# Optimization experiments

Hardware: AMD Instinct MI355X
Metric: run time of the kernel (lower is better)

## Reference

```python
import jax, jax.numpy as jnp
import numpy as np

TMSG = 15  # max_len - 1


def setup_inputs() -> dict:
    key = jax.random.key(0)
    ks = jax.random.split(key, 8)
    B, T_in, E, H, V = 4096, 4, 256, 512, 32000
    s = lambda k, shape: jax.random.normal(k, shape, jnp.float32) * 0.05
    return {
        "inp": jax.random.normal(ks[0], (B, T_in, E), jnp.float32),
        "Wx0": s(ks[1], (E, 4 * H)),
        "Wh0": s(ks[2], (H, 4 * H)),
        "b0": jnp.zeros((4 * H,), jnp.float32),
        "Wx1": s(ks[3], (H, 4 * H)),
        "Wh1": s(ks[4], (H, 4 * H)),
        "b1": jnp.zeros((4 * H,), jnp.float32),
        "Wd": s(ks[5], (H, V)),
        "bd": jnp.zeros((V,), jnp.float32),
    }


def _lstm_step(x, h, c, Wx, Wh, b):
    # Keras LSTMCell gate order: i, f, g(cell), o
    z = x @ Wx + h @ Wh + b
    i, f, g, o = jnp.split(z, 4, axis=-1)
    c = jax.nn.sigmoid(f) * c + jax.nn.sigmoid(i) * jnp.tanh(g)
    h = jax.nn.sigmoid(o) * jnp.tanh(c)
    return h, c


def reference(inp, Wx0, Wh0, b0, Wx1, Wh1, b1, Wd, bd):
    B = inp.shape[0]
    H = Wh0.shape[0]
    z = jnp.zeros((B, H), inp.dtype)

    def scan_fn(carry, x_t):
        h0, c0, h1, c1 = carry
        h0, c0 = _lstm_step(x_t, h0, c0, Wx0, Wh0, b0)
        h1, c1 = _lstm_step(h0, h1, c1, Wx1, Wh1, b1)
        return (h0, c0, h1, c1), None

    # NOTE: source bug resets initial_state to None every step, so each of the
    # max_len-1 steps runs the identical stacked LSTM from zero state; we run it once.
    (h0, c0, h1, c1), _ = jax.lax.scan(scan_fn, (z, z, z, z), jnp.swapaxes(inp, 0, 1))
    out = h1  # (B, H) last-step output of top cell

    log_probs = jax.nn.log_softmax(out @ Wd + bd, axis=-1)  # (B, V)
    probs = jnp.exp(log_probs)
    entropy = -jnp.sum(probs * log_probs, axis=-1)  # (B,)

    keys = jax.random.split(jax.random.key(42), TMSG)
    samples = jax.vmap(lambda k: jax.random.categorical(k, log_probs, axis=-1))(keys)  # (T, B)
    lp = log_probs[jnp.arange(B)[None, :], samples]  # (T, B) log_prob of sampled chars
    ent = jnp.broadcast_to(entropy[None], (TMSG, B))  # (T, B)

    message = samples.T  # (B, T)
    message = jnp.concatenate([message, jnp.zeros_like(message)], axis=1)  # (B, 2T)
    state_h = jnp.stack([h0, c0])  # keras unpack quirk: states[0] = [h, c] of cell 0
    return (message, lp, ent, state_h)
```

## Files before the change

### kernel.cpp

```cpp
#include <hip/hip_runtime.h>
#include <stdint.h>
#include <math.h>

#define BB 4096
#define HH 512
#define VV 32000
#define NT 15
#define STF 2097152
#define NXT 250

struct KeysArg { uint32_t w[2*NT]; };

__host__ __device__ inline void tf2x32(uint32_t k0, uint32_t k1,
                                       uint32_t x0, uint32_t x1,
                                       uint32_t& o0, uint32_t& o1) {
  uint32_t ks2 = k0 ^ k1 ^ 0x1BD11BDAu;
  x0 += k0; x1 += k1;
#define TF_R(r) { x0 += x1; x1 = (x1 << (r)) | (x1 >> (32 - (r))); x1 ^= x0; }
  TF_R(13) TF_R(15) TF_R(26) TF_R(6)
  x0 += k1; x1 += ks2 + 1u;
  TF_R(17) TF_R(29) TF_R(16) TF_R(24)
  x0 += ks2; x1 += k0 + 2u;
  TF_R(13) TF_R(15) TF_R(26) TF_R(6)
  x0 += k0; x1 += k1 + 3u;
  TF_R(17) TF_R(29) TF_R(16) TF_R(24)
  x0 += k1; x1 += ks2 + 4u;
  TF_R(13) TF_R(15) TF_R(26) TF_R(6)
  x0 += ks2; x1 += k0 + 5u;
#undef TF_R
  o0 = x0; o1 = x1;
}

__device__ inline void gll16(const float* g, float* l) {
  __builtin_amdgcn_global_load_lds(
      (const __attribute__((address_space(1))) void*)g,
      (__attribute__((address_space(3))) void*)l, 16, 0, 0);
}

__global__ __launch_bounds__(256)
void gemm_sk(const float* __restrict__ A0, int lda0,
             const float* __restrict__ W0, int koff0, int Klen0,
             const float* __restrict__ A1, int lda1,
             const float* __restrict__ W1, int koff1, int Klen1,
             int ldw,
             const float* __restrict__ bias,
             float* __restrict__ C0, float* __restrict__ C1, int ldc)
{
  const float* A; const float* W; float* C; int lda, koff, Klen;
  if (blockIdx.z == 0) { A = A0; lda = lda0; W = W0; koff = koff0; Klen = Klen0; C = C0; }
  else                 { A = A1; lda = lda1; W = W1; koff = koff1; Klen = Klen1; C = C1; }

  __shared__ float As[2][128 * 16];
  __shared__ float Ws[2][16 * 128];
  const int tid = threadIdx.x;
  const int lane = tid & 63, wv = tid >> 6;
  const int m0 = blockIdx.y * 128;
  const int n0 = blockIdx.x * 128;
  const int tx = tid & 15, ty = tid >> 4;

  float acc[8][8];
  #pragma unroll
  for (int i = 0; i < 8; ++i)
    #pragma unroll
    for (int j = 0; j < 8; ++j) acc[i][j] = 0.0f;

  const int a_row_in = (lane >> 2);
  const int a_chunk  = (lane & 3) * 4;
  const int w_row_in = (lane >> 5);
  const int w_col    = (lane & 31) * 4;

  auto STAGE = [&](int buf, int kt) {
    const int k0 = koff + (kt << 4);
    #pragma unroll
    for (int i = 0; i < 2; ++i) {
      const int seg = wv * 2 + i;
      gll16(A + (size_t)(m0 + seg * 16 + a_row_in) * lda + (k0 + a_chunk),
            &As[buf][seg * 256]);
      gll16(W + (size_t)(k0 + seg * 2 + w_row_in) * ldw + (n0 + w_col),
            &Ws[buf][seg * 256]);
    }
  };

  const int nkt = Klen >> 4;
  STAGE(0, 0);
  asm volatile("s_waitcnt vmcnt(0)" ::: "memory");
  __syncthreads();

  int cur = 0;
  for (int kt = 0; kt < nkt; ++kt) {
    if (kt + 1 < nkt) STAGE(cur ^ 1, kt + 1);
    #pragma unroll
    for (int kk4 = 0; kk4 < 4; ++kk4) {
      float4 a4[8];
      #pragma unroll
      for (int mm = 0; mm < 8; ++mm)
        a4[mm] = *(const float4*)&As[cur][(ty * 8 + mm) * 16 + kk4 * 4];
      #pragma unroll
      for (int q = 0; q < 4; ++q) {
        const int kk = kk4 * 4 + q;
        float4 b0 = *(const float4*)&Ws[cur][kk * 128 + tx * 4];
        float4 b1 = *(const float4*)&Ws[cur][kk * 128 + tx * 4 + 64];
        float br[8] = {b0.x,b0.y,b0.z,b0.w,b1.x,b1.y,b1.z,b1.w};
        #pragma unroll
        for (int mm = 0; mm < 8; ++mm) {
          float av = (q == 0) ? a4[mm].x : (q == 1) ? a4[mm].y
                   : (q == 2) ? a4[mm].z : a4[mm].w;
          #pragma unroll
          for (int j = 0; j < 8; ++j)
            acc[mm][j] = fmaf(av, br[j], acc[mm][j]);
        }
      }
    }
    asm volatile("s_waitcnt vmcnt(0)" ::: "memory");
    __syncthreads();
    cur ^= 1;
  }

  const int wn = tx * 4;
  #pragma unroll
  for (int i = 0; i < 8; ++i) {
    const int m = m0 + ty * 8 + i;
    float* dst = C + (size_t)m * ldc + (n0 + wn);
    float4 o0, o1;
    o0.x = acc[i][0]; o0.y = acc[i][1]; o0.z = acc[i][2]; o0.w = acc[i][3];
    o1.x = acc[i][4]; o1.y = acc[i][5]; o1.z = acc[i][6]; o1.w = acc[i][7];
    if (bias) {
      o0.x += bias[n0+wn+0]; o0.y += bias[n0+wn+1];
      o0.z += bias[n0+wn+2]; o0.w += bias[n0+wn+3];
      o1.x += bias[n0+wn+64]; o1.y += bias[n0+wn+65];
      o1.z += bias[n0+wn+66]; o1.w += bias[n0+wn+67];
    }
    *(float4*)dst        = o0;
    *(float4*)(dst + 64) = o1;
  }
}

__global__ __launch_bounds__(256)
void gate_kernel(const float* __restrict__ z0, const float* __restrict__ z1,
                 const float* __restrict__ bias,
                 const float* __restrict__ cin,
                 float* __restrict__ hout, float* __restrict__ cout,
                 float* __restrict__ sh, float* __restrict__ sc)
{
  int idx = blockIdx.x * 256 + threadIdx.x;
  int b = idx >> 9, j = idx & 511;
  const size_t r2 = (size_t)b * 2048;
  float zi = z0[r2+j]      + z1[r2+j]      + bias[j];
  float zf = z0[r2+j+512]  + z1[r2+j+512]  + bias[j+512];
  float zg = z0[r2+j+1024] + z1[r2+j+1024] + bias[j+1024];
  float zo = z0[r2+j+1536] + z1[r2+j+1536] + bias[j+1536];
  float si = 1.0f/(1.0f+expf(-zi));
  float sf = 1.0f/(1.0f+expf(-zf));
  float so = 1.0f/(1.0f+expf(-zo));
  float c = sf * cin[idx] + si * tanhf(zg);
  float h = so * tanhf(c);
  cout[idx] = c; hout[idx] = h;
  if (sh) { sh[idx] = h; sc[idx] = c; }
}

__global__ __launch_bounds__(256)
void rowstat_kernel(const float* __restrict__ logits,
                    float* __restrict__ rowM, float* __restrict__ rowLS,
                    float* __restrict__ rowEnt)
{
  const int row = blockIdx.x;
  const float* x = logits + (size_t)row * VV;
  const int tid = threadIdx.x;
  float m = -INFINITY;
  for (int v = tid; v < VV; v += 256) m = fmaxf(m, x[v]);
  #pragma unroll
  for (int off = 32; off; off >>= 1) m = fmaxf(m, __shfl_down(m, off));
  __shared__ float sm[4], ssum[4], swsum[4];
  if ((tid & 63) == 0) sm[tid >> 6] = m;
  __syncthreads();
  m = fmaxf(fmaxf(sm[0], sm[1]), fmaxf(sm[2], sm[3]));
  float s = 0.0f, w = 0.0f;
  for (int v = tid; v < VV; v += 256) {
    float d = x[v] - m;
    float e = expf(d);
    s += e; w += d * e;
  }
  #pragma unroll
  for (int off = 32; off; off >>= 1) { s += __shfl_down(s, off); w += __shfl_down(w, off); }
  if ((tid & 63) == 0) { ssum[tid >> 6] = s; swsum[tid >> 6] = w; }
  __syncthreads();
  if (tid == 0) {
    s = ssum[0]+ssum[1]+ssum[2]+ssum[3];
    w = swsum[0]+swsum[1]+swsum[2]+swsum[3];
    float ls = logf(s);
    rowM[row] = m; rowLS[row] = ls; rowEnt[row] = ls - w / s;
  }
}

__global__ __launch_bounds__(256)
void fused_sg(const float* __restrict__ logitsS,
              const float* __restrict__ rowM, const float* __restrict__ rowLS,
              const float* __restrict__ rowEnt,
              float* __restrict__ out, KeysArg keys, int bbaseS, int SB,
              const float* __restrict__ AG, const float* __restrict__ Wd,
              const float* __restrict__ bd, float* __restrict__ logitsG)
{
  __shared__ float As[2][128 * 16];
  __shared__ float Ws[2][16 * 128];
  __shared__ float rv[NT][4];
  __shared__ uint32_t ri[NT][4];

  const int tid = threadIdx.x;

  if ((int)blockIdx.x < SB) {
    const int l = blockIdx.x;
    const int b = bbaseS + l;
    const float* x = logitsS + (size_t)l * VV;
    const float m = rowM[l], ls = rowLS[l];

    float bv[NT];
    uint32_t bi[NT];
    float thr[NT];
    #pragma unroll
    for (int t = 0; t < NT; ++t) { bv[t] = -INFINITY; bi[t] = 0; thr[t] = 1.0f; }

    const uint32_t pbase = (uint32_t)b * (uint32_t)VV;
    for (int v = tid; v < VV; v += 256) {
      const float lp = (x[v] - m) - ls;
      const uint32_t p = pbase + (uint32_t)v;
      #pragma unroll
      for (int t = 0; t < NT; ++t) {
        uint32_t o0, o1;
        tf2x32(keys.w[2*t], keys.w[2*t+1], 0u, p, o0, o1);
        const uint32_t bits = o0 ^ o1;
        const float uf = __uint_as_float((bits >> 9) | 0x3f800000u);
        if (__any(uf >= thr[t])) {
          float u = fmaxf(uf - 1.0f, 1.17549435e-38f);
          float g = -logf(-logf(u)) + lp;
          bool improved = (uf >= thr[t]) && (g > bv[t]);
          if (improved) { bv[t] = g; bi[t] = (uint32_t)v; }
          if (__any(improved)) {
            float wb = bv[t];
            #pragma unroll
            for (int off = 1; off < 64; off <<= 1)
              wb = fmaxf(wb, __shfl_xor(wb, off));
            float us = expf(-expf(-(wb + ls)));
            thr[t] = 1.0f + us * 0.999999f;
          }
        }
      }
    }

    const int lane = tid & 63, wq = tid >> 6;
    #pragma unroll
    for (int t = 0; t < NT; ++t) {
      float v = bv[t]; uint32_t idx = bi[t];
      #pragma unroll
      for (int off = 32; off; off >>= 1) {
        float ov = __shfl_down(v, off);
        uint32_t oi = __shfl_down(idx, off);
        if (ov > v || (ov == v && oi < idx)) { v = ov; idx = oi; }
      }
      if (lane == 0) { rv[t][wq] = v; ri[t][wq] = idx; }
    }
    __syncthreads();
    if (tid < NT) {
      const int t = tid;
      float v = rv[t][0]; uint32_t idx = ri[t][0];
      #pragma unroll
      for (int q = 1; q < 4; ++q) {
        float ov = rv[t][q]; uint32_t oi = ri[t][q];
        if (ov > v || (ov == v && oi < idx)) { v = ov; idx = oi; }
      }
      out[(size_t)b * 30 + t]      = (float)idx;
      out[(size_t)b * 30 + 15 + t] = 0.0f;
      out[122880 + (size_t)t * BB + b] = (x[idx] - m) - ls;
      out[184320 + (size_t)t * BB + b] = rowEnt[l];
    }
    return;
  }

  const int gb = (int)blockIdx.x - SB;
  const int m0 = (gb / NXT) * 128;
  const int n0 = (gb % NXT) * 128;
  const int lane = tid & 63, wv = tid >> 6;
  const int tx = tid & 15, ty = tid >> 4;

  float acc[8][8];
  #pragma unroll
  for (int i = 0; i < 8; ++i)
    #pragma unroll
    for (int j = 0; j < 8; ++j) acc[i][j] = 0.0f;

  const int a_row_in = (lane >> 2);
  const int a_chunk  = (lane & 3) * 4;
  const int w_row_in = (lane >> 5);
  const int w_col    = (lane & 31) * 4;

  auto STAGE = [&](int buf, int kt) {
    const int k0 = kt << 4;
    #pragma unroll
    for (int i = 0; i < 2; ++i) {
      const int seg = wv * 2 + i;
      gll16(AG + (size_t)(m0 + seg * 16 + a_row_in) * 512 + (k0 + a_chunk),
            &As[buf][seg * 256]);
      gll16(Wd + (size_t)(k0 + seg * 2 + w_row_in) * VV + (n0 + w_col),
            &Ws[buf][seg * 256]);
    }
  };

  STAGE(0, 0);
  asm volatile("s_waitcnt vmcnt(0)" ::: "memory");
  __syncthreads();

  int cur = 0;
  for (int kt = 0; kt < 32; ++kt) {
    if (kt + 1 < 32) STAGE(cur ^ 1, kt + 1);
    #pragma unroll
    for (int kk4 = 0; kk4 < 4; ++kk4) {
      float4 a4[8];
      #pragma unroll
      for (int mm = 0; mm < 8; ++mm)
        a4[mm] = *(const float4*)&As[cur][(ty * 8 + mm) * 16 + kk4 * 4];
      #pragma unroll
      for (int q = 0; q < 4; ++q) {
        const int kk = kk4 * 4 + q;
        float4 b0 = *(const float4*)&Ws[cur][kk * 128 + tx * 4];
        float4 b1 = *(const float4*)&Ws[cur][kk * 128 + tx * 4 + 64];
        float br[8] = {b0.x,b0.y,b0.z,b0.w,b1.x,b1.y,b1.z,b1.w};
        #pragma unroll
        for (int mm = 0; mm < 8; ++mm) {
          float av = (q == 0) ? a4[mm].x : (q == 1) ? a4[mm].y
                   : (q == 2) ? a4[mm].z : a4[mm].w;
          #pragma unroll
          for (int j = 0; j < 8; ++j)
            acc[mm][j] = fmaf(av, br[j], acc[mm][j]);
        }
      }
    }
    asm volatile("s_waitcnt vmcnt(0)" ::: "memory");
    __syncthreads();
    cur ^= 1;
  }

  const int wn = tx * 4;
  #pragma unroll
  for (int i = 0; i < 8; ++i) {
    float* dst = logitsG + (size_t)(m0 + ty * 8 + i) * VV + (n0 + wn);
    float4 o0, o1;
    o0.x = acc[i][0] + bd[n0+wn+0];  o0.y = acc[i][1] + bd[n0+wn+1];
    o0.z = acc[i][2] + bd[n0+wn+2];  o0.w = acc[i][3] + bd[n0+wn+3];
    o1.x = acc[i][4] + bd[n0+wn+64]; o1.y = acc[i][5] + bd[n0+wn+65];
    o1.z = acc[i][6] + bd[n0+wn+66]; o1.w = acc[i][7] + bd[n0+wn+67];
    *(float4*)dst        = o0;
    *(float4*)(dst + 64) = o1;
  }
}

extern "C" void kernel_launch(void* const* d_in, const int* in_sizes, int n_in,
                              void* d_out, int out_size, void* d_ws, size_t ws_size,
                              hipStream_t stream)
{
  const float* inp = (const float*)d_in[0];
  const float* Wx0 = (const float*)d_in[1];
  const float* Wh0 = (const float*)d_in[2];
  const float* b0v = (const float*)d_in[3];
  const float* Wx1 = (const float*)d_in[4];
  const float* Wh1 = (const float*)d_in[5];
  const float* b1v = (const float*)d_in[6];
  const float* Wd  = (const float*)d_in[7];
  const float* bdv = (const float*)d_in[8];
  float* out = (float*)d_out;
  float* ws = (float*)d_ws;

  float* h0 = ws;
  float* c0 = ws + (size_t)STF;
  float* h1 = ws + (size_t)2*STF;
  float* c1 = ws + (size_t)3*STF;
  float* rowM0  = ws + (size_t)4*STF;
  float* rowLS0 = rowM0 + 1024;
  float* rowEnt0 = rowLS0 + 1024;
  float* rowM1  = rowEnt0 + 1024;
  float* rowLS1 = rowM1 + 1024;
  float* rowEnt1 = rowLS1 + 1024;
  float* region = ws + (size_t)4*STF + 12288;
  float* z0 = region;
  float* z1 = region + (size_t)4096*2048;

  size_t ws_floats = ws_size / 4;
  size_t base = (size_t)4*STF + 12288;
  int CH = 512;
  while (CH > 128 && base + (size_t)2*CH*VV > ws_floats) CH >>= 1;
  float* logitsA = region;
  float* logitsB = region + (size_t)CH*VV;

  hipMemsetAsync(ws, 0, (size_t)4*STF*sizeof(float), stream);

  for (int t = 0; t < 4; ++t) {
    gemm_sk<<<dim3(2048/128, 4096/128, 2), 256, 0, stream>>>(
        h0, 512, Wh0, 0, 512,
        inp + t*256, 1024, Wx0, 0, 256,
        2048, nullptr, z0, z1, 2048);
    gate_kernel<<<STF/256, 256, 0, stream>>>(
        z0, z1, b0v, c0, h0, c0,
        (t==3) ? out + 245760 : (float*)nullptr,
        (t==3) ? out + 245760 + STF : (float*)nullptr);
    gemm_sk<<<dim3(2048/128, 4096/128, 2), 256, 0, stream>>>(
        h0, 512, Wx1, 0, 512,
        h1, 512, Wh1, 0, 512,
        2048, nullptr, z0, z1, 2048);
    gate_kernel<<<STF/256, 256, 0, stream>>>(
        z0, z1, b1v, c1, h1, c1, (float*)nullptr, (float*)nullptr);
  }

  KeysArg ka;
  for (int t = 0; t < NT; ++t) {
    uint32_t o0, o1;
    tf2x32(0u, 42u, 0u, (uint32_t)t, o0, o1);
    ka.w[2*t] = o0; ka.w[2*t+1] = o1;
  }

  const int nch = 4096 / CH;
  const int GB = NXT * (CH / 128);

  fused_sg<<<GB, 256, 0, stream>>>(
      nullptr, nullptr, nullptr, nullptr, out, ka, 0, 0,
      h1, Wd, bdv, logitsA);
  rowstat_kernel<<<CH, 256, 0, stream>>>(logitsA, rowM0, rowLS0, rowEnt0);

  for (int c = 0; c < nch; ++c) {
    float* lgS = (c & 1) ? logitsB : logitsA;
    float* lgG = (c & 1) ? logitsA : logitsB;
    float* rM = (c & 1) ? rowM1 : rowM0;
    float* rL = (c & 1) ? rowLS1 : rowLS0;
    float* rE = (c & 1) ? rowEnt1 : rowEnt0;
    const bool more = (c + 1 < nch);
    fused_sg<<<CH + (more ? GB : 0), 256, 0, stream>>>(
        lgS, rM, rL, rE, out, ka, c * CH, CH,
        more ? (h1 + (size_t)(c + 1) * CH * 512) : h1, Wd, bdv, lgG);
    if (more) {
      float* rM2 = (c & 1) ? rowM0 : rowM1;
      float* rL2 = (c & 1) ? rowLS0 : rowLS1;
      float* rE2 = (c & 1) ? rowEnt0 : rowEnt1;
      rowstat_kernel<<<CH, 256, 0, stream>>>(lgG, rM2, rL2, rE2);
    }
  }
}
```

Before: 7.216 ms.

## Fuse row softmax stats into sampling blocks and swizzle A-tile LDS layout

Removes the separate rowstat kernel and computes the row max, log-sum-exp and entropy inside the sampling blocks of fused_sg, cutting one launch per chunk and the round trip of row statistics through global memory. It also XOR-swizzles the 16-float chunk placement of the A tile in LDS in both GEMMs, so the float4 reads by different ty groups hit different banks. The trade-off is that sampling blocks now read each logits row two extra times plus the sampling pass, and the stats work is no longer overlapped as a separate kernel.

After: 7.417 ms. +2.8%, slower.

```diff
diff --git a/kernel.cpp b/kernel.cpp
--- a/kernel.cpp
+++ b/kernel.cpp
@@ -37,6 +37,7 @@
       (__attribute__((address_space(3))) void*)l, 16, 0, 0);
 }
 
+
 __global__ __launch_bounds__(256)
 void gemm_sk(const float* __restrict__ A0, int lda0,
              const float* __restrict__ W0, int koff0, int Klen0,
@@ -65,15 +66,17 @@
     for (int j = 0; j < 8; ++j) acc[i][j] = 0.0f;
 
   const int a_row_in = (lane >> 2);
-  const int a_chunk  = (lane & 3) * 4;
   const int w_row_in = (lane >> 5);
   const int w_col    = (lane & 31) * 4;
+  const int tys      = ty & 3;
 
   auto STAGE = [&](int buf, int kt) {
     const int k0 = koff + (kt << 4);
     #pragma unroll
     for (int i = 0; i < 2; ++i) {
       const int seg = wv * 2 + i;
+      const int s = (seg * 2 + (lane >> 5)) & 3;
+      const int a_chunk = ((lane & 3) ^ s) * 4;
       gll16(A + (size_t)(m0 + seg * 16 + a_row_in) * lda + (k0 + a_chunk),
             &As[buf][seg * 256]);
       gll16(W + (size_t)(k0 + seg * 2 + w_row_in) * ldw + (n0 + w_col),
@@ -91,10 +94,11 @@
     if (kt + 1 < nkt) STAGE(cur ^ 1, kt + 1);
     #pragma unroll
     for (int kk4 = 0; kk4 < 4; ++kk4) {
+      const int cs = (kk4 ^ tys) * 4;
       float4 a4[8];
       #pragma unroll
       for (int mm = 0; mm < 8; ++mm)
-        a4[mm] = *(const float4*)&As[cur][(ty * 8 + mm) * 16 + kk4 * 4];
+        a4[mm] = *(const float4*)&As[cur][(ty * 8 + mm) * 16 + cs];
       #pragma unroll
       for (int q = 0; q < 4; ++q) {
         const int kk = kk4 * 4 + q;
@@ -159,43 +163,7 @@
 }
 
 __global__ __launch_bounds__(256)
-void rowstat_kernel(const float* __restrict__ logits,
-                    float* __restrict__ rowM, float* __restrict__ rowLS,
-                    float* __restrict__ rowEnt)
-{
-  const int row = blockIdx.x;
-  const float* x = logits + (size_t)row * VV;
-  const int tid = threadIdx.x;
-  float m = -INFINITY;
-  for (int v = tid; v < VV; v += 256) m = fmaxf(m, x[v]);
-  #pragma unroll
-  for (int off = 32; off; off >>= 1) m = fmaxf(m, __shfl_down(m, off));
-  __shared__ float sm[4], ssum[4], swsum[4];
-  if ((tid & 63) == 0) sm[tid >> 6] = m;
-  __syncthreads();
-  m = fmaxf(fmaxf(sm[0], sm[1]), fmaxf(sm[2], sm[3]));
-  float s = 0.0f, w = 0.0f;
-  for (int v = tid; v < VV; v += 256) {
-    float d = x[v] - m;
-    float e = expf(d);
-    s += e; w += d * e;
-  }
-  #pragma unroll
-  for (int off = 32; off; off >>= 1) { s += __shfl_down(s, off); w += __shfl_down(w, off); }
-  if ((tid & 63) == 0) { ssum[tid >> 6] = s; swsum[tid >> 6] = w; }
-  __syncthreads();
-  if (tid == 0) {
-    s = ssum[0]+ssum[1]+ssum[2]+ssum[3];
-    w = swsum[0]+swsum[1]+swsum[2]+swsum[3];
-    float ls = logf(s);
-    rowM[row] = m; rowLS[row] = ls; rowEnt[row] = ls - w / s;
-  }
-}
-
-__global__ __launch_bounds__(256)
 void fused_sg(const float* __restrict__ logitsS,
-              const float* __restrict__ rowM, const float* __restrict__ rowLS,
-              const float* __restrict__ rowEnt,
               float* __restrict__ out, KeysArg keys, int bbaseS, int SB,
               const float* __restrict__ AG, const float* __restrict__ Wd,
               const float* __restrict__ bd, float* __restrict__ logitsG)
@@ -204,6 +172,7 @@
   __shared__ float Ws[2][16 * 128];
   __shared__ float rv[NT][4];
   __shared__ uint32_t ri[NT][4];
+  __shared__ float sm[4], ssum[4], swsum[4], sbc[2];
 
   const int tid = threadIdx.x;
 
@@ -211,7 +180,32 @@
     const int l = blockIdx.x;
     const int b = bbaseS + l;
     const float* x = logitsS + (size_t)l * VV;
-    const float m = rowM[l], ls = rowLS[l];
+
+    float m = -INFINITY;
+    for (int v = tid; v < VV; v += 256) m = fmaxf(m, x[v]);
+    #pragma unroll
+    for (int off = 32; off; off >>= 1) m = fmaxf(m, __shfl_down(m, off));
+    if ((tid & 63) == 0) sm[tid >> 6] = m;
+    __syncthreads();
+    m = fmaxf(fmaxf(sm[0], sm[1]), fmaxf(sm[2], sm[3]));
+    float s = 0.0f, w = 0.0f;
+    for (int v = tid; v < VV; v += 256) {
+      float d = x[v] - m;
+      float e = expf(d);
+      s += e; w += d * e;
+    }
+    #pragma unroll
+    for (int off = 32; off; off >>= 1) { s += __shfl_down(s, off); w += __shfl_down(w, off); }
+    if ((tid & 63) == 0) { ssum[tid >> 6] = s; swsum[tid >> 6] = w; }
+    __syncthreads();
+    if (tid == 0) {
+      s = ssum[0]+ssum[1]+ssum[2]+ssum[3];
+      w = swsum[0]+swsum[1]+swsum[2]+swsum[3];
+      float ls0 = logf(s);
+      sbc[0] = ls0; sbc[1] = ls0 - w / s;
+    }
+    __syncthreads();
+    const float ls = sbc[0], ent = sbc[1];
 
     float bv[NT];
     uint32_t bi[NT];
@@ -270,7 +264,7 @@
       out[(size_t)b * 30 + t]      = (float)idx;
       out[(size_t)b * 30 + 15 + t] = 0.0f;
       out[122880 + (size_t)t * BB + b] = (x[idx] - m) - ls;
-      out[184320 + (size_t)t * BB + b] = rowEnt[l];
+      out[184320 + (size_t)t * BB + b] = ent;
     }
     return;
   }
@@ -288,15 +282,17 @@
     for (int j = 0; j < 8; ++j) acc[i][j] = 0.0f;
 
   const int a_row_in = (lane >> 2);
-  const int a_chunk  = (lane & 3) * 4;
   const int w_row_in = (lane >> 5);
   const int w_col    = (lane & 31) * 4;
+  const int tys      = ty & 3;
 
   auto STAGE = [&](int buf, int kt) {
     const int k0 = kt << 4;
     #pragma unroll
     for (int i = 0; i < 2; ++i) {
       const int seg = wv * 2 + i;
+      const int s = (seg * 2 + (lane >> 5)) & 3;
+      const int a_chunk = ((lane & 3) ^ s) * 4;
       gll16(AG + (size_t)(m0 + seg * 16 + a_row_in) * 512 + (k0 + a_chunk),
             &As[buf][seg * 256]);
       gll16(Wd + (size_t)(k0 + seg * 2 + w_row_in) * VV + (n0 + w_col),
@@ -313,10 +309,11 @@
     if (kt + 1 < 32) STAGE(cur ^ 1, kt + 1);
     #pragma unroll
     for (int kk4 = 0; kk4 < 4; ++kk4) {
+      const int cs = (kk4 ^ tys) * 4;
       float4 a4[8];
       #pragma unroll
       for (int mm = 0; mm < 8; ++mm)
-        a4[mm] = *(const float4*)&As[cur][(ty * 8 + mm) * 16 + kk4 * 4];
+        a4[mm] = *(const float4*)&As[cur][(ty * 8 + mm) * 16 + cs];
       #pragma unroll
       for (int q = 0; q < 4; ++q) {
         const int kk = kk4 * 4 + q;
@@ -372,12 +369,6 @@
   float* c0 = ws + (size_t)STF;
   float* h1 = ws + (size_t)2*STF;
   float* c1 = ws + (size_t)3*STF;
-  float* rowM0  = ws + (size_t)4*STF;
-  float* rowLS0 = rowM0 + 1024;
-  float* rowEnt0 = rowLS0 + 1024;
-  float* rowM1  = rowEnt0 + 1024;
-  float* rowLS1 = rowM1 + 1024;
-  float* rowEnt1 = rowLS1 + 1024;
   float* region = ws + (size_t)4*STF + 12288;
   float* z0 = region;
   float* z1 = region + (size_t)4096*2048;
@@ -419,25 +410,14 @@
   const int GB = NXT * (CH / 128);
 
   fused_sg<<<GB, 256, 0, stream>>>(
-      nullptr, nullptr, nullptr, nullptr, out, ka, 0, 0,
-      h1, Wd, bdv, logitsA);
-  rowstat_kernel<<<CH, 256, 0, stream>>>(logitsA, rowM0, rowLS0, rowEnt0);
+      nullptr, out, ka, 0, 0, h1, Wd, bdv, logitsA);
 
   for (int c = 0; c < nch; ++c) {
     float* lgS = (c & 1) ? logitsB : logitsA;
     float* lgG = (c & 1) ? logitsA : logitsB;
-    float* rM = (c & 1) ? rowM1 : rowM0;
-    float* rL = (c & 1) ? rowLS1 : rowLS0;
-    float* rE = (c & 1) ? rowEnt1 : rowEnt0;
     const bool more = (c + 1 < nch);
     fused_sg<<<CH + (more ? GB : 0), 256, 0, stream>>>(
-        lgS, rM, rL, rE, out, ka, c * CH, CH,
+        lgS, out, ka, c * CH, CH,
         more ? (h1 + (size_t)(c + 1) * CH * 512) : h1, Wd, bdv, lgG);
-    if (more) {
-      float* rM2 = (c & 1) ? rowM0 : rowM1;
-      float* rL2 = (c & 1) ? rowLS0 : rowLS1;
-      float* rE2 = (c & 1) ? rowEnt0 : rowEnt1;
-      rowstat_kernel<<<CH, 256, 0, stream>>>(lgG, rM2, rL2, rE2);
-    }
-  }
-}
+  }
+}
```

## Split sampling rows across two blocks by vocab half and combine partial argmaxes

Applied to the files above, without the earlier changes.

Each sampling row is now processed by two blocks, each covering half of the vocabulary. Each block writes its per-step best value and index to a workspace buffer, and a new combine kernel picks the winner and writes the outputs. This doubles sampling parallelism to cut the tail of the fused sample/GEMM launch, at the cost of an extra kernel launch per chunk and some workspace. On equal values across the two halves the lower index wins (v1 > v0 picks the second half only when strictly greater), which preserves the original tie-break.

Measured after the change: 7.311 ms. No clear change (+1.3%).

```diff
diff --git a/kernel.cpp b/kernel.cpp
--- a/kernel.cpp
+++ b/kernel.cpp
@@ -8,6 +8,7 @@
 #define NT 15
 #define STF 2097152
 #define NXT 250
+#define VSPLIT 16128
 
 struct KeysArg { uint32_t w[2*NT]; };
 
@@ -198,7 +199,8 @@
               const float* __restrict__ rowEnt,
               float* __restrict__ out, KeysArg keys, int bbaseS, int SB,
               const float* __restrict__ AG, const float* __restrict__ Wd,
-              const float* __restrict__ bd, float* __restrict__ logitsG)
+              const float* __restrict__ bd, float* __restrict__ logitsG,
+              float* __restrict__ pv, uint32_t* __restrict__ pi)
 {
   __shared__ float As[2][128 * 16];
   __shared__ float Ws[2][16 * 128];
@@ -208,10 +210,13 @@
   const int tid = threadIdx.x;
 
   if ((int)blockIdx.x < SB) {
-    const int l = blockIdx.x;
+    const int l = blockIdx.x >> 1;
+    const int h = blockIdx.x & 1;
     const int b = bbaseS + l;
     const float* x = logitsS + (size_t)l * VV;
     const float m = rowM[l], ls = rowLS[l];
+    const int vbeg = h ? VSPLIT : 0;
+    const int vend = h ? VV : VSPLIT;
 
     float bv[NT];
     uint32_t bi[NT];
@@ -220,7 +225,7 @@
     for (int t = 0; t < NT; ++t) { bv[t] = -INFINITY; bi[t] = 0; thr[t] = 1.0f; }
 
     const uint32_t pbase = (uint32_t)b * (uint32_t)VV;
-    for (int v = tid; v < VV; v += 256) {
+    for (int v = vbeg + tid; v < vend; v += 256) {
       const float lp = (x[v] - m) - ls;
       const uint32_t p = pbase + (uint32_t)v;
       #pragma unroll
@@ -267,10 +272,8 @@
         float ov = rv[t][q]; uint32_t oi = ri[t][q];
         if (ov > v || (ov == v && oi < idx)) { v = ov; idx = oi; }
       }
-      out[(size_t)b * 30 + t]      = (float)idx;
-      out[(size_t)b * 30 + 15 + t] = 0.0f;
-      out[122880 + (size_t)t * BB + b] = (x[idx] - m) - ls;
-      out[184320 + (size_t)t * BB + b] = rowEnt[l];
+      pv[(size_t)(l * NT + t) * 2 + h] = v;
+      pi[(size_t)(l * NT + t) * 2 + h] = idx;
     }
     return;
   }
@@ -352,6 +355,28 @@
   }
 }
 
+__global__ __launch_bounds__(64)
+void combine_kernel(const float* __restrict__ logits,
+                    const float* __restrict__ rowM, const float* __restrict__ rowLS,
+                    const float* __restrict__ rowEnt,
+                    const float* __restrict__ pv, const uint32_t* __restrict__ pi,
+                    float* __restrict__ out, int bbase)
+{
+  const int l = blockIdx.x;
+  const int t = threadIdx.x;
+  if (t >= NT) return;
+  const size_t e = (size_t)(l * NT + t) * 2;
+  float v0 = pv[e], v1 = pv[e + 1];
+  uint32_t idx = (v1 > v0) ? pi[e + 1] : pi[e];
+  const int b = bbase + l;
+  const float* x = logits + (size_t)l * VV;
+  const float m = rowM[l], ls = rowLS[l];
+  out[(size_t)b * 30 + t]      = (float)idx;
+  out[(size_t)b * 30 + 15 + t] = 0.0f;
+  out[122880 + (size_t)t * BB + b] = (x[idx] - m) - ls;
+  out[184320 + (size_t)t * BB + b] = rowEnt[l];
+}
+
 extern "C" void kernel_launch(void* const* d_in, const int* in_sizes, int n_in,
                               void* d_out, int out_size, void* d_ws, size_t ws_size,
                               hipStream_t stream)
@@ -385,9 +410,11 @@
   size_t ws_floats = ws_size / 4;
   size_t base = (size_t)4*STF + 12288;
   int CH = 512;
-  while (CH > 128 && base + (size_t)2*CH*VV > ws_floats) CH >>= 1;
+  while (CH > 128 && base + (size_t)2*CH*VV + (size_t)4*CH*NT > ws_floats) CH >>= 1;
   float* logitsA = region;
   float* logitsB = region + (size_t)CH*VV;
+  float* pv = region + (size_t)2*CH*VV;
+  uint32_t* pi = (uint32_t*)(pv + (size_t)CH*NT*2);
 
   hipMemsetAsync(ws, 0, (size_t)4*STF*sizeof(float), stream);
 
@@ -420,7 +447,7 @@
 
   fused_sg<<<GB, 256, 0, stream>>>(
       nullptr, nullptr, nullptr, nullptr, out, ka, 0, 0,
-      h1, Wd, bdv, logitsA);
+      h1, Wd, bdv, logitsA, nullptr, nullptr);
   rowstat_kernel<<<CH, 256, 0, stream>>>(logitsA, rowM0, rowLS0, rowEnt0);
 
   for (int c = 0; c < nch; ++c) {
@@ -430,9 +457,10 @@
     float* rL = (c & 1) ? rowLS1 : rowLS0;
     float* rE = (c & 1) ? rowEnt1 : rowEnt0;
     const bool more = (c + 1 < nch);
-    fused_sg<<<CH + (more ? GB : 0), 256, 0, stream>>>(
-        lgS, rM, rL, rE, out, ka, c * CH, CH,
-        more ? (h1 + (size_t)(c + 1) * CH * 512) : h1, Wd, bdv, lgG);
+    fused_sg<<<2*CH + (more ? GB : 0), 256, 0, stream>>>(
+        lgS, rM, rL, rE, out, ka, c * CH, 2*CH,
+        more ? (h1 + (size_t)(c + 1) * CH * 512) : h1, Wd, bdv, lgG, pv, pi);
+    combine_kernel<<<CH, 64, 0, stream>>>(lgS, rM, rL, rE, pv, pi, out, c * CH);
     if (more) {
       float* rM2 = (c & 1) ? rowM0 : rowM1;
       float* rL2 = (c & 1) ? rowLS0 : rowLS1;
```
